# Kernel optimization log

Hardware: AMD Instinct MI355X
Metric: run time of the kernel (lower is better)

Reference implementation:

```python
import jax, jax.numpy as jnp
import numpy as np

# Dims (match init_kwargs / input_specs)
N, N_REP, K, D = 8, 2048, 16, 3
C_IN, C_LIFT = 64, 64
C_MID = C_IN + C_LIFT   # 128
C_OUT = 128             # groups=C_OUT -> depthwise since C_MID == C_OUT
EPS = 1e-5


def setup_inputs() -> dict:
    key = jax.random.key(0)
    ks = jax.random.split(key, 10)
    w = lambda i, shape, fan_in: (jax.random.uniform(ks[i], shape, dtype=jnp.float32) * 2.0 - 1.0) / np.float32(np.sqrt(fan_in))
    return dict(
        p=jax.random.normal(ks[0], (N, N_REP, D), dtype=jnp.float32),
        P=jax.random.normal(ks[1], (N, N_REP, K, D), dtype=jnp.float32),
        F=jax.random.normal(ks[2], (N, N_REP, K, C_IN), dtype=jnp.float32),
        # BatchNorm over the D spatial channels (training-mode stats)
        bn_gamma=jnp.ones((D,), dtype=jnp.float32),
        bn_beta=jnp.zeros((D,), dtype=jnp.float32),
        # mlp_lift: Dense(D->C_LIFT) + Dense(C_LIFT->C_LIFT), ELU each
        lift_w1=w(3, (D, C_LIFT), D), lift_b1=jnp.zeros((C_LIFT,), dtype=jnp.float32),
        lift_w2=w(4, (C_LIFT, C_LIFT), C_LIFT), lift_b2=jnp.zeros((C_LIFT,), dtype=jnp.float32),
        # mid_conv: 1x1 Conv2d(D -> K) channels-last == Linear on last dim
        mid_w=w(5, (D, K), D), mid_b=jnp.zeros((K,), dtype=jnp.float32),
        # mlp: Dense(K->K) with ELU
        mlp_w=w(6, (K, K), K), mlp_b=jnp.zeros((K,), dtype=jnp.float32),
        # end_conv: Conv2d(C_MID -> C_OUT, kernel (K,1), groups=C_OUT) == depthwise
        # reduction over the neighbor dim; weight per (out_channel, neighbor)
        end_w=w(7, (C_OUT, K), K), end_b=jnp.zeros((C_OUT,), dtype=jnp.float32),
    )


def reference(p, P, F, bn_gamma, bn_beta, lift_w1, lift_b1, lift_w2, lift_b2,
              mid_w, mid_b, mlp_w, mlp_b, end_w, end_b):
    # Center neighborhoods on the representative point
    P_local = P - p[:, :, None, :]                              # (N,R,K,D)
    # Channels-last BatchNorm over D, batch stats over (N,R,K)
    mean = jnp.mean(P_local, axis=(0, 1, 2), keepdims=True)
    var = jnp.var(P_local, axis=(0, 1, 2), keepdims=True)
    P_norm = (P_local - mean) * jax.lax.rsqrt(var + EPS) * bn_gamma + bn_beta
    # Lift spatial coords to C_LIFT features (MLP of Dense+ELU layers)
    F_lift = jax.nn.elu(P_norm @ lift_w1 + lift_b1)
    F_lift = jax.nn.elu(F_lift @ lift_w2 + lift_b2)             # (N,R,K,C_LIFT)
    F_cat = jnp.concatenate([F_lift, F], axis=-1)               # (N,R,K,C_MID)
    # X-transform: 1x1 conv D->K then Dense(K->K)+ELU -> (N,R,K,K)
    X = P_norm @ mid_w + mid_b
    X = jax.nn.elu(X @ mlp_w + mlp_b)
    # Weighted aggregation: small batched matmul over the neighbor dim
    F_X = jnp.einsum('nrkj,nrjc->nrkc', X, F_cat)               # (N,R,K,C_MID)
    # Depthwise end conv: per-channel weighted sum over neighbors
    F_p = jnp.einsum('nrkc,ck->nrc', F_X, end_w) + end_b        # (N,R,C_OUT)
    return F_p
```

## Files before the change

### kernel.cpp

```cpp
#include <hip/hip_runtime.h>
#include <cstddef>

#define N_TOT   8
#define R_TOT   2048
#define NR_TOT  (N_TOT*R_TOT)
#define KK      16
#define CL      64
#define CM      128
#define EPSV    1e-5f
#define CNTF    262144.0f

typedef float  f32x4  __attribute__((ext_vector_type(4)));
typedef short  bf16x8 __attribute__((ext_vector_type(8)));

union FragU { bf16x8 f; unsigned u[4]; };

__device__ __forceinline__ float elu_f(float x){
    return x > 0.f ? x : (__expf(x) - 1.f);
}

#if defined(__has_builtin) && __has_builtin(__builtin_amdgcn_cvt_pk_bf16_f32)
__device__ __forceinline__ unsigned pk_bf16(float a, float b){
    auto v = __builtin_amdgcn_cvt_pk_bf16_f32(a, b);
    unsigned u; __builtin_memcpy(&u, &v, 4);
    return u;
}
#else
__device__ __forceinline__ unsigned pk_bf16(float a, float b){
    unsigned ua = __float_as_uint(a), ub = __float_as_uint(b);
    ua += 0x7fff + ((ua >> 16) & 1);
    ub += 0x7fff + ((ub >> 16) & 1);
    return (ua >> 16) | (ub & 0xffff0000u);
}
#endif
__device__ __forceinline__ float bf_lo(unsigned u){ return __uint_as_float(u << 16); }
__device__ __forceinline__ float bf_hi(unsigned u){ return __uint_as_float(u & 0xffff0000u); }

__device__ __forceinline__ void split4(const float* x, unsigned* o){
    unsigned h01 = pk_bf16(x[0], x[1]);
    unsigned h23 = pk_bf16(x[2], x[3]);
    float l0 = x[0] - bf_lo(h01), l1 = x[1] - bf_hi(h01);
    float l2 = x[2] - bf_lo(h23), l3 = x[3] - bf_hi(h23);
    o[0] = h01; o[1] = h23; o[2] = pk_bf16(l0, l1); o[3] = pk_bf16(l2, l3);
}

__global__ __launch_bounds__(256) void xconv_stats(
    const float* __restrict__ p, const float* __restrict__ P, float* __restrict__ ws)
{
    float s1[3] = {0.f,0.f,0.f}, s2[3] = {0.f,0.f,0.f};
    const int total = NR_TOT * KK;
    for (int idx = blockIdx.x*256 + threadIdx.x; idx < total; idx += gridDim.x*256){
        int nr = idx >> 4;
        #pragma unroll
        for (int d = 0; d < 3; d++){
            float v = P[idx*3 + d] - p[nr*3 + d];
            s1[d] += v;
            s2[d] += v*v;
        }
    }
    #pragma unroll
    for (int off = 32; off > 0; off >>= 1){
        #pragma unroll
        for (int d = 0; d < 3; d++){
            s1[d] += __shfl_down(s1[d], off, 64);
            s2[d] += __shfl_down(s2[d], off, 64);
        }
    }
    __shared__ float red[4][6];
    int wave = threadIdx.x >> 6, lane = threadIdx.x & 63;
    if (lane == 0){
        #pragma unroll
        for (int d = 0; d < 3; d++){ red[wave][d] = s1[d]; red[wave][3+d] = s2[d]; }
    }
    __syncthreads();
    if (threadIdx.x < 6){
        float a = red[0][threadIdx.x] + red[1][threadIdx.x]
                + red[2][threadIdx.x] + red[3][threadIdx.x];
        atomicAdd(&ws[threadIdx.x], a);
    }
}

__global__ __launch_bounds__(256) void xconv_main(
    const float* __restrict__ p,   const float* __restrict__ P,
    const float* __restrict__ F,
    const float* __restrict__ gamma,const float* __restrict__ beta,
    const float* __restrict__ w1,  const float* __restrict__ b1,
    const float* __restrict__ w2,  const float* __restrict__ b2,
    const float* __restrict__ midw,const float* __restrict__ midb,
    const float* __restrict__ mlpw,const float* __restrict__ mlpb,
    const float* __restrict__ endw,const float* __restrict__ endb,
    const float* __restrict__ ws,  float* __restrict__ out)
{
    __shared__ float sEndw[128*20];

    const int tid  = threadIdx.x;
    const int lane = tid & 63;
    const int lo16 = lane & 15;
    const int quad = lane >> 4;
    const int wave = tid >> 6;

    {
        const float4* ep = (const float4*)endw;
        float4 v0 = ep[tid*2], v1 = ep[tid*2 + 1];
        int c = tid >> 1, k0 = (tid & 1) * 8;
        float* dst = &sEndw[c*20 + k0];
        *(float4*)dst = v0; *(float4*)(dst + 4) = v1;
    }
    __syncthreads();

    float sc[3], sh[3];
    #pragma unroll
    for (int d = 0; d < 3; d++){
        float mean = ws[d] / CNTF;
        float var  = ws[3+d] / CNTF - mean*mean;
        float s    = gamma[d] * rsqrtf(var + EPSV);
        sc[d] = s; sh[d] = beta[d] - mean*s;
    }

    unsigned w1pk[2][8][2];
    #pragma unroll
    for (int s = 0; s < 2; s++)
        #pragma unroll
        for (int j = 0; j < 8; j++){
            int q = s*32 + quad*8 + j;
            w1pk[s][j][0] = pk_bf16(w1[q],        w1[64 + q]);
            w1pk[s][j][1] = pk_bf16(w1[128 + q],  b1[q]);
        }
    FragU w2f[4][2];
    #pragma unroll
    for (int b = 0; b < 4; b++)
        #pragma unroll
        for (int s = 0; s < 2; s++)
            #pragma unroll
            for (int d = 0; d < 4; d++){
                int q0 = s*32 + quad*8 + d*2;
                int idx = q0*64 + b*16 + lo16;
                w2f[b][s].u[d] = pk_bf16(w2[idx], w2[idx + 64]);
            }
    FragU mlpA[2];
    {
        float mw[4];
        #pragma unroll
        for (int r = 0; r < 4; r++) mw[r] = mlpw[(quad*4 + r)*16 + lo16];
        unsigned o[4]; split4(mw, o);
        mlpA[0].u[0]=o[0]; mlpA[0].u[1]=o[1]; mlpA[0].u[2]=o[0]; mlpA[0].u[3]=o[1];
        mlpA[1].u[0]=o[2]; mlpA[1].u[1]=o[3]; mlpA[1].u[2]=o[2]; mlpA[1].u[3]=o[3];
    }
    float mlpbr[4];
    #pragma unroll
    for (int r = 0; r < 4; r++) mlpbr[r] = mlpb[quad*4 + r];
    float mw0[4], mw1[4], mw2[4], mbv[4];
    #pragma unroll
    for (int j = 0; j < 4; j++){
        int m2 = quad*4 + j;
        mw0[j] = midw[m2]; mw1[j] = midw[16 + m2]; mw2[j] = midw[32 + m2];
        mbv[j] = midb[m2];
    }
    float b2r[4];
    #pragma unroll
    for (int b = 0; b < 4; b++) b2r[b] = b2[b*16 + lo16];
    const float endb0 = endb[lane], endb1 = endb[64 + lane];

    const int wglobal = blockIdx.x*4 + wave;

    #pragma unroll 1
    for (int it = 0; it < 4; it++){
        const int nr = wglobal*4 + it;

        const int pb = nr*48 + lo16*3;
        float P0 = P[pb], P1 = P[pb+1], P2 = P[pb+2];
        float pp0 = p[nr*3], pp1 = p[nr*3+1], pp2 = p[nr*3+2];
        float fv[4][4];
        #pragma unroll
        for (int bt = 0; bt < 4; bt++)
            #pragma unroll
            for (int r = 0; r < 4; r++)
                fv[bt][r] = F[(size_t)nr*1024 + (quad*4 + r)*64 + bt*16 + lo16];

        const float pn0 = (P0 - pp0)*sc[0] + sh[0];
        const float pn1 = (P1 - pp1)*sc[1] + sh[1];
        const float pn2 = (P2 - pp2)*sc[2] + sh[2];

        FragU hf[2];
        #pragma unroll
        for (int s = 0; s < 2; s++)
            #pragma unroll
            for (int d = 0; d < 4; d++){
                float e[2];
                #pragma unroll
                for (int h2 = 0; h2 < 2; h2++){
                    unsigned pa = w1pk[s][2*d + h2][0], pbk = w1pk[s][2*d + h2][1];
                    float h = bf_hi(pbk);
                    h = fmaf(pn0, bf_lo(pa), h);
                    h = fmaf(pn1, bf_hi(pa), h);
                    h = fmaf(pn2, bf_lo(pbk), h);
                    e[h2] = elu_f(h);
                }
                hf[s].u[d] = pk_bf16(e[0], e[1]);
            }

        float x0[4];
        #pragma unroll
        for (int j = 0; j < 4; j++)
            x0[j] = fmaf(pn2, mw2[j], fmaf(pn1, mw1[j], fmaf(pn0, mw0[j], mbv[j])));
        FragU x0f; split4(x0, x0f.u);

        f32x4 dx = {0.f,0.f,0.f,0.f};
        dx = __builtin_amdgcn_mfma_f32_16x16x32_bf16(mlpA[0].f, x0f.f, dx, 0,0,0);
        dx = __builtin_amdgcn_mfma_f32_16x16x32_bf16(mlpA[1].f, x0f.f, dx, 0,0,0);
        float xv[4];
        #pragma unroll
        for (int r = 0; r < 4; r++) xv[r] = elu_f(dx[r] + mlpbr[r]);
        FragU xA; split4(xv, xA.u);

        float o0 = 0.f, o1 = 0.f;

        #pragma unroll
        for (int b = 0; b < 4; b++){
            f32x4 dl = {0.f,0.f,0.f,0.f};
            dl = __builtin_amdgcn_mfma_f32_16x16x32_bf16(hf[0].f, w2f[b][0].f, dl, 0,0,0);
            dl = __builtin_amdgcn_mfma_f32_16x16x32_bf16(hf[1].f, w2f[b][1].f, dl, 0,0,0);
            float fl[4];
            #pragma unroll
            for (int r = 0; r < 4; r++) fl[r] = elu_f(dl[r] + b2r[b]);
            FragU bfg;
            unsigned h01 = pk_bf16(fl[0], fl[1]), h23 = pk_bf16(fl[2], fl[3]);
            bfg.u[0] = h01; bfg.u[1] = h23; bfg.u[2] = h01; bfg.u[3] = h23;
            f32x4 da = {0.f,0.f,0.f,0.f};
            da = __builtin_amdgcn_mfma_f32_16x16x32_bf16(xA.f, bfg.f, da, 0,0,0);
            const float4 ew = *(const float4*)&sEndw[(b*16 + lo16)*20 + quad*4];
            float pt = da[0]*ew.x + da[1]*ew.y + da[2]*ew.z + da[3]*ew.w;
            pt += __shfl_xor(pt, 16, 64);
            pt += __shfl_xor(pt, 32, 64);
            if (b == quad) o0 = pt;
        }
        #pragma unroll
        for (int bt = 0; bt < 4; bt++){
            FragU bfg;
            unsigned h01 = pk_bf16(fv[bt][0], fv[bt][1]);
            unsigned h23 = pk_bf16(fv[bt][2], fv[bt][3]);
            bfg.u[0] = h01; bfg.u[1] = h23; bfg.u[2] = h01; bfg.u[3] = h23;
            f32x4 da = {0.f,0.f,0.f,0.f};
            da = __builtin_amdgcn_mfma_f32_16x16x32_bf16(xA.f, bfg.f, da, 0,0,0);
            const float4 ew = *(const float4*)&sEndw[(64 + bt*16 + lo16)*20 + quad*4];
            float pt = da[0]*ew.x + da[1]*ew.y + da[2]*ew.z + da[3]*ew.w;
            pt += __shfl_xor(pt, 16, 64);
            pt += __shfl_xor(pt, 32, 64);
            if (bt == quad) o1 = pt;
        }

        out[(size_t)nr*CM + lane]      = o0 + endb0;
        out[(size_t)nr*CM + 64 + lane] = o1 + endb1;
    }
}

extern "C" void kernel_launch(void* const* d_in, const int* in_sizes, int n_in,
                              void* d_out, int out_size, void* d_ws, size_t ws_size,
                              hipStream_t stream)
{
    const float* p     = (const float*)d_in[0];
    const float* P     = (const float*)d_in[1];
    const float* F     = (const float*)d_in[2];
    const float* gamma = (const float*)d_in[3];
    const float* beta  = (const float*)d_in[4];
    const float* w1    = (const float*)d_in[5];
    const float* b1    = (const float*)d_in[6];
    const float* w2    = (const float*)d_in[7];
    const float* b2    = (const float*)d_in[8];
    const float* midw  = (const float*)d_in[9];
    const float* midb  = (const float*)d_in[10];
    const float* mlpw  = (const float*)d_in[11];
    const float* mlpb  = (const float*)d_in[12];
    const float* endw  = (const float*)d_in[13];
    const float* endb  = (const float*)d_in[14];
    float* ws  = (float*)d_ws;
    float* out = (float*)d_out;

    hipMemsetAsync(d_ws, 0, 32, stream);
    xconv_stats<<<256, 256, 0, stream>>>(p, P, ws);
    xconv_main <<<1024, 256, 0, stream>>>(p, P, F, gamma, beta, w1, b1, w2, b2,
                                          midw, midb, mlpw, mlpb, endw, endb, ws, out);
}
```

Measured before the change: 148.3 us.

## Vectorize BN stats loads and prefetch next point coords in main loop

The stats kernel drops its grid-stride loop: each thread now loads twelve floats of P as three float4 loads and reduces four neighbors in registers. This correctly covers the input only if the host launches exactly the matching number of blocks. The main kernel software-pipelines the per-iteration P and p loads by fetching the next representative's coordinates while the current one is processed, to hide global load latency. That costs a few extra registers.

```diff
diff --git a/kernel.cpp b/kernel.cpp
--- a/kernel.cpp
+++ b/kernel.cpp
@@ -47,17 +47,19 @@
 __global__ __launch_bounds__(256) void xconv_stats(
     const float* __restrict__ p, const float* __restrict__ P, float* __restrict__ ws)
 {
-    float s1[3] = {0.f,0.f,0.f}, s2[3] = {0.f,0.f,0.f};
-    const int total = NR_TOT * KK;
-    for (int idx = blockIdx.x*256 + threadIdx.x; idx < total; idx += gridDim.x*256){
-        int nr = idx >> 4;
-        #pragma unroll
-        for (int d = 0; d < 3; d++){
-            float v = P[idx*3 + d] - p[nr*3 + d];
-            s1[d] += v;
-            s2[d] += v*v;
-        }
-    }
+    const int g = blockIdx.x*256 + threadIdx.x;
+    const float4* P4 = (const float4*)(P + (size_t)g*12);
+    float4 a = P4[0], b = P4[1], c = P4[2];
+    const int nr = g >> 2;
+    float pp0 = p[nr*3], pp1 = p[nr*3+1], pp2 = p[nr*3+2];
+    float vx0=a.x-pp0, vx1=a.w-pp0, vx2=b.z-pp0, vx3=c.y-pp0;
+    float vy0=a.y-pp1, vy1=b.x-pp1, vy2=b.w-pp1, vy3=c.z-pp1;
+    float vz0=a.z-pp2, vz1=b.y-pp2, vz2=c.x-pp2, vz3=c.w-pp2;
+    float s1[3], s2[3];
+    s1[0]=vx0+vx1+vx2+vx3; s2[0]=vx0*vx0+vx1*vx1+vx2*vx2+vx3*vx3;
+    s1[1]=vy0+vy1+vy2+vy3; s2[1]=vy0*vy0+vy1*vy1+vy2*vy2+vy3*vy3;
+    s1[2]=vz0+vz1+vz2+vz3; s2[2]=vz0*vz0+vz1*vz1+vz2*vz2+vz3*vz3;
+
     #pragma unroll
     for (int off = 32; off > 0; off >>= 1){
         #pragma unroll
@@ -74,9 +76,9 @@
     }
     __syncthreads();
     if (threadIdx.x < 6){
-        float a = red[0][threadIdx.x] + red[1][threadIdx.x]
+        float v = red[0][threadIdx.x] + red[1][threadIdx.x]
                 + red[2][threadIdx.x] + red[3][threadIdx.x];
-        atomicAdd(&ws[threadIdx.x], a);
+        atomicAdd(&ws[threadIdx.x], v);
     }
 }
 
@@ -163,19 +165,34 @@
 
     const int wglobal = blockIdx.x*4 + wave;
 
+    float nP0, nP1, nP2, npp0, npp1, npp2;
+    {
+        const int nr0 = wglobal*4;
+        const int pb  = nr0*48 + lo16*3;
+        nP0 = P[pb]; nP1 = P[pb+1]; nP2 = P[pb+2];
+        npp0 = p[nr0*3]; npp1 = p[nr0*3+1]; npp2 = p[nr0*3+2];
+    }
+
     #pragma unroll 1
     for (int it = 0; it < 4; it++){
         const int nr = wglobal*4 + it;
 
-        const int pb = nr*48 + lo16*3;
-        float P0 = P[pb], P1 = P[pb+1], P2 = P[pb+2];
-        float pp0 = p[nr*3], pp1 = p[nr*3+1], pp2 = p[nr*3+2];
+        const float P0 = nP0, P1 = nP1, P2 = nP2;
+        const float pp0 = npp0, pp1 = npp1, pp2 = npp2;
+
         float fv[4][4];
         #pragma unroll
         for (int bt = 0; bt < 4; bt++)
             #pragma unroll
             for (int r = 0; r < 4; r++)
                 fv[bt][r] = F[(size_t)nr*1024 + (quad*4 + r)*64 + bt*16 + lo16];
+
+        if (it < 3){
+            const int nn = nr + 1;
+            const int pb = nn*48 + lo16*3;
+            nP0 = P[pb]; nP1 = P[pb+1]; nP2 = P[pb+2];
+            npp0 = p[nn*3]; npp1 = p[nn*3+1]; npp2 = p[nn*3+2];
+        }
 
         const float pn0 = (P0 - pp0)*sc[0] + sh[0];
         const float pn1 = (P1 - pp1)*sc[1] + sh[1];
```

Result: no change. 147.7 us (-0.4%).
